# Optimization experiments

Measured on AMD Instinct MI355X. Metric: run time of the kernel, lower is better.

## Reference

```python
import jax, jax.numpy as jnp
import numpy as np

B, C, H, W = 4, 256, 128, 128
HEADS, KD, VD = 8, 64, 64
EPS = 1e-5


def setup_inputs() -> dict:
    key = jax.random.key(0)
    ks = jax.random.split(key, 5)
    s = 0.02
    return {
        "x": jax.random.normal(ks[0], (B, C, H, W), dtype=jnp.float32),
        "wq": jax.random.normal(ks[1], (HEADS * KD, C), dtype=jnp.float32) * s,
        "bq": jnp.zeros((HEADS * KD,), dtype=jnp.float32),
        "wk": jax.random.normal(ks[2], (HEADS * KD, C), dtype=jnp.float32) * s,
        "bk": jnp.zeros((HEADS * KD,), dtype=jnp.float32),
        "wv": jax.random.normal(ks[3], (HEADS * VD, C), dtype=jnp.float32) * s,
        "bv": jnp.zeros((HEADS * VD,), dtype=jnp.float32),
        "wo": jax.random.normal(ks[4], (C, HEADS * VD), dtype=jnp.float32) * s,
        "bo": jnp.zeros((C,), dtype=jnp.float32),
        "g_q": jnp.ones((KD,), dtype=jnp.float32),
        "be_q": jnp.zeros((KD,), dtype=jnp.float32),
        "g_k": jnp.ones((KD,), dtype=jnp.float32),
        "be_k": jnp.zeros((KD,), dtype=jnp.float32),
        "g_v": jnp.ones((VD,), dtype=jnp.float32),
        "be_v": jnp.zeros((VD,), dtype=jnp.float32),
    }


def _conv1x1(t, w, b):
    # t: [B,C,H,W], w: [O,C] -> [B,O,H,W]
    return jnp.einsum("bchw,oc->bohw", t, w) + b[None, :, None, None]


def _ln_dim(t, g, be):
    # LayerNorm over the per-head feature axis (axis=2) of [B,heads,dim,N]
    mu = jnp.mean(t, axis=2, keepdims=True)
    var = jnp.var(t, axis=2, keepdims=True)
    return (t - mu) * jax.lax.rsqrt(var + EPS) * g[None, None, :, None] + be[None, None, :, None]


def reference(x, wq, bq, wk, bk, wv, bv, wo, bo, g_q, be_q, g_k, be_k, g_v, be_v):
    b, c, h, w = x.shape
    n = h * w
    # context defaults to x
    q = _conv1x1(x, wq, bq).reshape(b, HEADS, KD, n)
    k = _conv1x1(x, wk, bk).reshape(b, HEADS, KD, n)
    v = _conv1x1(x, wv, bv).reshape(b, HEADS, VD, n)
    q = _ln_dim(q, g_q, be_q)
    k = _ln_dim(k, g_k, be_k)
    v = _ln_dim(v, g_v, be_v)
    q = jax.nn.softmax(q * (KD ** -0.25), axis=2)  # softmax over key_dim
    k = jax.nn.softmax(k, axis=3)                  # softmax over N
    ctx = jnp.einsum("bhkn,bhvn->bhkv", k, v)      # [B,heads,KD,VD]
    out = jnp.einsum("bhkn,bhkv->bhvn", q, ctx)    # [B,heads,VD,N]
    out = out.reshape(b, HEADS * VD, h, w)
    return _conv1x1(out, wo, bo)
```

## Files before the change

### kernel.cpp

```cpp
#include <hip/hip_runtime.h>
#include <hip/hip_bf16.h>
#include <stdint.h>

typedef unsigned short u16;
typedef __attribute__((__vector_size__(16))) short s16x8;
typedef __attribute__((__vector_size__(16))) float f32x4;

#define N_ 16384
#define C_ 256

__device__ __forceinline__ float bf2f(u16 u) {
    union { uint32_t i; float f; } v; v.i = ((uint32_t)u) << 16; return v.f;
}
__device__ __forceinline__ u16 f2bf(float f) {
    union { uint32_t i; float f; } v; v.f = f;
    uint32_t u = v.i;
    return (u16)((u + 0x7FFFu + ((u >> 16) & 1u)) >> 16);
}

__device__ __forceinline__ void gl_lds16(const u16* g, u16* l) {
    __builtin_amdgcn_global_load_lds((__attribute__((address_space(1))) void*)g,
                                     (__attribute__((address_space(3))) void*)l,
                                     16, 0, 0);
}

__global__ __launch_bounds__(256) void transpose_kernel(const float* __restrict__ x,
                                                        u16* __restrict__ xT) {
    __shared__ float T[64][65];
    int tid = threadIdx.x;
    int n0 = blockIdx.x * 64, c0 = blockIdx.y * 64, b = blockIdx.z;
    const float* xp = x + (size_t)b * C_ * N_;
    for (int it = 0; it < 16; it++) {
        int idx = it * 256 + tid;
        int c = idx >> 6, n = idx & 63;
        T[c][n] = xp[(size_t)(c0 + c) * N_ + n0 + n];
    }
    __syncthreads();
    u16* op = xT + (size_t)b * N_ * C_;
    for (int it = 0; it < 8; it++) {
        int idx = it * 256 + tid;
        int n = idx >> 5, c2 = (idx & 31) * 2;
        uint32_t lo = f2bf(T[c2][n]);
        uint32_t hi = f2bf(T[c2 + 1][n]);
        *(uint32_t*)&op[(size_t)(n0 + n) * C_ + c0 + c2] = lo | (hi << 16);
    }
}

__global__ __launch_bounds__(256) void cvtw_kernel(const float* __restrict__ wq,
                                                   const float* __restrict__ wk,
                                                   const float* __restrict__ wv,
                                                   u16* __restrict__ wb,
                                                   float* __restrict__ rs) {
    int m = blockIdx.y;
    if (m == 0 && blockIdx.x < 8) rs[blockIdx.x * 256 + threadIdx.x] = 0.f;
    const float* s = m == 0 ? wq : (m == 1 ? wk : wv);
    int i = blockIdx.x * 256 + threadIdx.x;
    wb[(size_t)m * 131072 + i] = f2bf(s[i]);
}


__global__ __launch_bounds__(256) void kvctx_kernel(
    const u16* __restrict__ xT, const u16* __restrict__ wb,
    const float* __restrict__ bk, const float* __restrict__ bv,
    const float* __restrict__ gk, const float* __restrict__ bek,
    const float* __restrict__ gv, const float* __restrict__ bev,
    float* __restrict__ ctxp, float* __restrict__ rs)
{
    __shared__ u16 SH[4][8704];
    int tid = threadIdx.x;
    int lane = tid & 63, wid = tid >> 6;
    int quad = lane >> 4, l15 = lane & 15;
    int wm = wid >> 1, wn = wid & 1;
    int ns = blockIdx.x, h = blockIdx.y, b = blockIdx.z;

    const u16* wsrcw = wb + (size_t)(1 + (wid >> 1)) * 131072
                          + ((size_t)h * 64 + (size_t)(wid & 1) * 32) * 256;

    int srow = lane >> 3;
    int sc8  = ((lane & 7) ^ srow) * 8;

#define STAGEF(XP, KC, CUR) {                                                      \
    int koff_ = (KC) * 64 + sc8;                                                   \
    _Pragma("unroll")                                                              \
    for (int i_ = 0; i_ < 4; i_++) {                                               \
        int ri_ = i_ * 8 + srow;                                                   \
        gl_lds16(&wsrcw[(size_t)ri_ * 256 + koff_], &SH[CUR][(wid * 4 + i_) * 512]); \
        gl_lds16(&(XP)[(size_t)(wid * 32 + ri_) * 256 + koff_], &SH[2 + (CUR)][(wid * 4 + i_) * 512]); \
    } }

    const float* bptr  = wm ? bv  : bk;
    const float* gptr  = wm ? gv  : gk;
    const float* beptr = wm ? bev : bek;
    float bB_[4], gB[4], eB[4];
#pragma unroll
    for (int nf = 0; nf < 4; nf++) {
        int rl = nf * 16 + l15;
        bB_[nf] = bptr[h * 64 + rl];
        gB[nf]  = gptr[rl];
        eB[nf]  = beptr[rl];
    }

    f32x4 cacc[4][4];
#pragma unroll
    for (int i = 0; i < 4; i++)
#pragma unroll
        for (int j = 0; j < 4; j++) cacc[i][j] = (f32x4){0.f, 0.f, 0.f, 0.f};
    float rs_acc[4] = {0.f, 0.f, 0.f, 0.f};

    {
        const u16* x0 = xT + ((size_t)b * N_ + (size_t)(ns * 8) * 128) * 256;
        STAGEF(x0, 0, 0);
    }
    __syncthreads();

    for (int t = 0; t < 8; t++) {
        const u16* xcur = xT + ((size_t)b * N_ + (size_t)(ns * 8 + t) * 128) * 256;

        f32x4 acc[4][4];
#pragma unroll
        for (int i = 0; i < 4; i++)
#pragma unroll
            for (int j = 0; j < 4; j++) acc[i][j] = (f32x4){0.f, 0.f, 0.f, 0.f};

        for (int kc = 0; kc < 4; kc++) {
            int cur = (kc + t) & 1;
            if (kc < 3) STAGEF(xcur, kc + 1, cur ^ 1);
            const u16* Wb = &SH[cur][0];
            const u16* Xb = &SH[2 + cur][0];
#pragma unroll
            for (int ks = 0; ks < 2; ks++) {
                int cc = ks * 4 + quad;
                s16x8 af[4], bf[4];
#pragma unroll
                for (int f = 0; f < 4; f++) {
                    int ar = wn * 64 + f * 16 + l15;
                    int br = wm * 64 + f * 16 + l15;
                    af[f] = *(const s16x8*)&Xb[ar * 64 + ((cc ^ (ar & 7)) * 8)];
                    bf[f] = *(const s16x8*)&Wb[br * 64 + ((cc ^ (br & 7)) * 8)];
                }
#pragma unroll
                for (int i = 0; i < 4; i++)
#pragma unroll
                    for (int j = 0; j < 4; j++)
                        acc[i][j] = __builtin_amdgcn_mfma_f32_16x16x32_bf16(af[i], bf[j], acc[i][j], 0, 0, 0);
            }
            if (kc < 3) __syncthreads();
        }

#pragma unroll
        for (int mf = 0; mf < 4; mf++)
#pragma unroll
            for (int nf = 0; nf < 4; nf++)
#pragma unroll
                for (int r = 0; r < 4; r++) acc[mf][nf][r] += bB_[nf];
        float sa[4][4], sb[4][4];
#pragma unroll
        for (int mf = 0; mf < 4; mf++)
#pragma unroll
            for (int r = 0; r < 4; r++) {
                float s = 0.f, s2 = 0.f;
#pragma unroll
                for (int nf = 0; nf < 4; nf++) { float v = acc[mf][nf][r]; s += v; s2 += v * v; }
                sa[mf][r] = s; sb[mf][r] = s2;
            }
#pragma unroll
        for (int msk = 1; msk <= 8; msk <<= 1)
#pragma unroll
            for (int mf = 0; mf < 4; mf++)
#pragma unroll
                for (int r = 0; r < 4; r++) {
                    sa[mf][r] += __shfl_xor(sa[mf][r], msk);
                    sb[mf][r] += __shfl_xor(sb[mf][r], msk);
                }
#pragma unroll
        for (int mf = 0; mf < 4; mf++)
#pragma unroll
            for (int r = 0; r < 4; r++) {
                float mu = sa[mf][r] * (1.f / 64.f);
                float rstd = rsqrtf(sb[mf][r] * (1.f / 64.f) - mu * mu + 1e-5f);
#pragma unroll
                for (int nf = 0; nf < 4; nf++)
                    acc[mf][nf][r] = (acc[mf][nf][r] - mu) * rstd * gB[nf] + eB[nf];
            }
        if (wm == 0) {
#pragma unroll
            for (int mf = 0; mf < 4; mf++)
#pragma unroll
                for (int nf = 0; nf < 4; nf++)
#pragma unroll
                    for (int r = 0; r < 4; r++) acc[mf][nf][r] = __expf(acc[mf][nf][r]);
#pragma unroll
            for (int nf = 0; nf < 4; nf++) {
                float s = 0.f;
#pragma unroll
                for (int mf = 0; mf < 4; mf++)
#pragma unroll
                    for (int r = 0; r < 4; r++) s += acc[mf][nf][r];
                s += __shfl_xor(s, 16); s += __shfl_xor(s, 32);
                rs_acc[nf] += s;
            }
        }

        int esb = t & 1;
        u16* ES = &SH[esb][0];
        u16* VS = &SH[2 + esb][0];
        {
            u16* st = wm ? VS : ES;
#pragma unroll
            for (int mf = 0; mf < 4; mf++)
#pragma unroll
                for (int nf = 0; nf < 4; nf++) {
                    int rh = nf * 16 + l15;
                    int ln = wn * 64 + mf * 16 + quad * 4;
                    int c  = ln >> 3;
                    int off = rh * 128 + ((c ^ (rh & 15)) * 8) + (ln & 7);
                    uint64_t w0 = (uint64_t)f2bf(acc[mf][nf][0]) | ((uint64_t)f2bf(acc[mf][nf][1]) << 16) |
                                  ((uint64_t)f2bf(acc[mf][nf][2]) << 32) | ((uint64_t)f2bf(acc[mf][nf][3]) << 48);
                    *(uint64_t*)&st[off] = w0;
                }
        }
        __syncthreads();

        if (t < 7) {
            const u16* xnext = xT + ((size_t)b * N_ + (size_t)(ns * 8 + t + 1) * 128) * 256;
            STAGEF(xnext, 0, (t + 1) & 1);
        }
        {
            int cc = wid * 4 + quad;
            s16x8 caf[4], cbf[4];
#pragma unroll
            for (int f = 0; f < 4; f++) {
                int off = (f * 16 + l15) * 128 + ((cc ^ l15) * 8);
                caf[f] = *(const s16x8*)&ES[off];
                cbf[f] = *(const s16x8*)&VS[off];
            }
#pragma unroll
            for (int i = 0; i < 4; i++)
#pragma unroll
                for (int j = 0; j < 4; j++)
                    cacc[i][j] = __builtin_amdgcn_mfma_f32_16x16x32_bf16(caf[i], cbf[j], cacc[i][j], 0, 0, 0);
        }
        __syncthreads();
    }

    if (wm == 0 && quad == 0) {
#pragma unroll
        for (int nf = 0; nf < 4; nf++)
            atomicAdd(&rs[(size_t)b * 512 + h * 64 + nf * 16 + l15], rs_acc[nf]);
    }
    {
        float* CTXW = (float*)((char*)SH + (size_t)wid * 17408);
#pragma unroll
        for (int mf = 0; mf < 4; mf++)
#pragma unroll
            for (int nf = 0; nf < 4; nf++) {
                int kd = mf * 16 + quad * 4, vd = nf * 16 + l15;
                *(f32x4*)&CTXW[vd * 68 + kd] = cacc[mf][nf];
            }
    }
    __syncthreads();
    {
        int vd = tid >> 2, kd0 = (tid & 3) * 16;
        const float* C0 = (const float*)((char*)SH);
        const float* C1 = (const float*)((char*)SH + 17408);
        const float* C2 = (const float*)((char*)SH + 34816);
        const float* C3 = (const float*)((char*)SH + 52224);
        float* gp = ctxp + (((size_t)(b * 8 + h) * 16 + ns) * 4096) + vd * 64 + kd0;
#pragma unroll
        for (int j4 = 0; j4 < 4; j4++) {
            int o = vd * 68 + kd0 + j4 * 4;
            f32x4 s = *(const f32x4*)&C0[o];
            s += *(const f32x4*)&C1[o];
            s += *(const f32x4*)&C2[o];
            s += *(const f32x4*)&C3[o];
            *(f32x4*)&gp[j4 * 4] = s;
        }
    }
#undef STAGEF
}

__global__ __launch_bounds__(256) void weff_kernel(
    const float* __restrict__ ctxp, const float* __restrict__ rs,
    const float* __restrict__ wo, u16* __restrict__ Weffb)
{
    __shared__ float CT[16][65];
    int tid = threadIdx.x;
    int h = blockIdx.x, b = blockIdx.y, kc = blockIdx.z;
    for (int i = tid; i < 1024; i += 256) {
        int kdl = i >> 6, vd = i & 63;
        int kd = kc * 16 + kdl;
        float s = 0.f;
#pragma unroll
        for (int sl = 0; sl < 16; sl++)
            s += ctxp[(((size_t)(b * 8 + h) * 16 + sl) * 4096) + vd * 64 + kd];
        CT[kdl][vd] = s / rs[(size_t)b * 512 + h * 64 + kd];
    }
    __syncthreads();
    int c = tid;
    float wrow[64];
    const float4* wp = (const float4*)(wo + (size_t)c * 512 + h * 64);
#pragma unroll
    for (int i = 0; i < 16; i++) { float4 t = wp[i]; wrow[i*4] = t.x; wrow[i*4+1] = t.y; wrow[i*4+2] = t.z; wrow[i*4+3] = t.w; }
    for (int kdl = 0; kdl < 16; kdl++) {
        float s = 0.f;
#pragma unroll
        for (int vd = 0; vd < 64; vd++) s += wrow[vd] * CT[kdl][vd];
        Weffb[((size_t)b * 256 + c) * 512 + h * 64 + kc * 16 + kdl] = f2bf(s);
    }
}

__global__ __launch_bounds__(256) void qout_kernel(
    const u16* __restrict__ xT, const u16* __restrict__ wb,
    const float* __restrict__ bq, const float* __restrict__ gq, const float* __restrict__ beq,
    const u16* __restrict__ Weffb, const float* __restrict__ bo, float* __restrict__ out)
{
    __shared__ u16 WS[2][8192];
    __shared__ u16 QB[2][8192];
    int tid = threadIdx.x;
    int lane = tid & 63, wid = tid >> 6;
    int quad = lane >> 4, l15 = lane & 15;
    int wm = wid >> 1, wn = wid & 1;
    int nt = blockIdx.x, b = blockIdx.y;
    int n0 = nt * 128;

    const u16* xsrc = xT + ((size_t)b * N_ + n0) * 256;
    int srow = lane >> 3;
    int sc8  = ((lane & 7) ^ srow) * 8;

    f32x4 oacc[8][4];
#pragma unroll
    for (int i = 0; i < 8; i++)
#pragma unroll
        for (int j = 0; j < 4; j++) oacc[i][j] = (f32x4){0.f, 0.f, 0.f, 0.f};

#define QSTAGE(WSRC, KC, CUR) {                                                    \
    int koff_ = (KC) * 64 + sc8;                                                   \
    _Pragma("unroll")                                                              \
    for (int i_ = 0; i_ < 4; i_++) {                                               \
        int row_ = (wid * 4 + i_) * 8 + srow;                                      \
        gl_lds16(&(WSRC)[(size_t)row_ * 256 + koff_], &WS[CUR][(wid * 4 + i_) * 512]);  \
        gl_lds16(&xsrc[(size_t)row_ * 256 + koff_], &QB[CUR][(wid * 4 + i_) * 512]);    \
    } }

    for (int p = 0; p < 4; p++) {
        const u16* wsrc = wb + (size_t)(p * 128) * 256;
        f32x4 qacc[4][4];
#pragma unroll
        for (int i = 0; i < 4; i++)
#pragma unroll
            for (int j = 0; j < 4; j++) qacc[i][j] = (f32x4){0.f, 0.f, 0.f, 0.f};

        QSTAGE(wsrc, 0, 0);
        __syncthreads();
        for (int kc = 0; kc < 4; kc++) {
            int cur = kc & 1;
            if (kc < 3) QSTAGE(wsrc, kc + 1, cur ^ 1);
            const u16* Wb = &WS[cur][0];
            const u16* Xb = &QB[cur][0];
#pragma unroll
            for (int ks = 0; ks < 2; ks++) {
                int cc = ks * 4 + quad;
                s16x8 af[4], bf[4];
#pragma unroll
                for (int f = 0; f < 4; f++) {
                    int ar = wm * 64 + f * 16 + l15;
                    int br = wn * 64 + f * 16 + l15;
                    af[f] = *(const s16x8*)&Wb[ar * 64 + ((cc ^ (ar & 7)) * 8)];
                    bf[f] = *(const s16x8*)&Xb[br * 64 + ((cc ^ (br & 7)) * 8)];
                }
#pragma unroll
                for (int i = 0; i < 4; i++)
#pragma unroll
                    for (int j = 0; j < 4; j++)
                        qacc[i][j] = __builtin_amdgcn_mfma_f32_16x16x32_bf16(af[i], bf[j], qacc[i][j], 0, 0, 0);
            }
            if (kc < 3) __syncthreads();
        }

        int r0 = p * 128;
        float bA[4][4], gA[4][4], eA[4][4];
#pragma unroll
        for (int mf = 0; mf < 4; mf++)
#pragma unroll
            for (int r = 0; r < 4; r++) {
                int rl = mf * 16 + quad * 4 + r;
                bA[mf][r] = bq[r0 + wm * 64 + rl];
                gA[mf][r] = gq[rl];
                eA[mf][r] = beq[rl];
            }
#pragma unroll
        for (int mf = 0; mf < 4; mf++)
#pragma unroll
            for (int nf = 0; nf < 4; nf++)
#pragma unroll
                for (int r = 0; r < 4; r++) qacc[mf][nf][r] += bA[mf][r];
#pragma unroll
        for (int nf = 0; nf < 4; nf++) {
            float s = 0.f, s2 = 0.f;
#pragma unroll
            for (int mf = 0; mf < 4; mf++)
#pragma unroll
                for (int r = 0; r < 4; r++) { float v = qacc[mf][nf][r]; s += v; s2 += v * v; }
            s  += __shfl_xor(s, 16);  s  += __shfl_xor(s, 32);
            s2 += __shfl_xor(s2, 16); s2 += __shfl_xor(s2, 32);
            float mu = s * (1.f / 64.f);
            float rstd = rsqrtf(s2 * (1.f / 64.f) - mu * mu + 1e-5f);
#pragma unroll
            for (int mf = 0; mf < 4; mf++)
#pragma unroll
                for (int r = 0; r < 4; r++)
                    qacc[mf][nf][r] = (qacc[mf][nf][r] - mu) * rstd * gA[mf][r] + eA[mf][r];
        }
        const float s_q = 0.35355339059327373f;
#pragma unroll
        for (int nf = 0; nf < 4; nf++) {
            float m = -1e30f;
#pragma unroll
            for (int mf = 0; mf < 4; mf++)
#pragma unroll
                for (int r = 0; r < 4; r++) { qacc[mf][nf][r] *= s_q; m = fmaxf(m, qacc[mf][nf][r]); }
            m = fmaxf(m, __shfl_xor(m, 16)); m = fmaxf(m, __shfl_xor(m, 32));
            float d = 0.f;
#pragma unroll
            for (int mf = 0; mf < 4; mf++)
#pragma unroll
                for (int r = 0; r < 4; r++) { float e = __expf(qacc[mf][nf][r] - m); qacc[mf][nf][r] = e; d += e; }
            d += __shfl_xor(d, 16); d += __shfl_xor(d, 32);
            float inv = 1.f / d;
#pragma unroll
            for (int mf = 0; mf < 4; mf++)
#pragma unroll
                for (int r = 0; r < 4; r++) qacc[mf][nf][r] *= inv;
        }
        __syncthreads();
        {
            u16* st = &QB[wn][0];
#pragma unroll
            for (int mf = 0; mf < 4; mf++)
#pragma unroll
                for (int nf = 0; nf < 4; nf++) {
                    int nl = nf * 16 + l15;
                    int gl = wm * 64 + mf * 16 + quad * 4;
                    int c  = gl >> 3;
                    int off = nl * 128 + ((c ^ (nl & 15)) * 8) + (gl & 7);
                    uint64_t w0 = (uint64_t)f2bf(qacc[mf][nf][0]) | ((uint64_t)f2bf(qacc[mf][nf][1]) << 16) |
                                  ((uint64_t)f2bf(qacc[mf][nf][2]) << 32) | ((uint64_t)f2bf(qacc[mf][nf][3]) << 48);
                    *(uint64_t*)&st[off] = w0;
                }
        }
        __syncthreads();

#pragma unroll
        for (int sub = 0; sub < 2; sub++) {
#pragma unroll
            for (int i_ = 0; i_ < 8; i_++) {
                int row = wid * 64 + i_ * 8 + srow;
                gl_lds16(&Weffb[((size_t)b * 256 + row) * 512 + p * 128 + sub * 64 + sc8],
                         &WS[wid >> 1][((wid & 1) * 64 + i_ * 8) * 64]);
            }
            __syncthreads();
#pragma unroll
            for (int ks = 0; ks < 2; ks++) {
                int cca = ks * 4 + quad;
                int ccb = sub * 8 + ks * 4 + quad;
                s16x8 af[8], bf[4];
#pragma unroll
                for (int f = 0; f < 8; f++) {
                    int ar = f * 16 + l15;
                    af[f] = *(const s16x8*)&WS[wm][ar * 64 + ((cca ^ (ar & 7)) * 8)];
                }
#pragma unroll
                for (int f = 0; f < 4; f++) {
                    int br = f * 16 + l15;
                    bf[f] = *(const s16x8*)&QB[wn][br * 128 + ((ccb ^ (br & 15)) * 8)];
                }
#pragma unroll
                for (int i = 0; i < 8; i++)
#pragma unroll
                    for (int j = 0; j < 4; j++)
                        oacc[i][j] = __builtin_amdgcn_mfma_f32_16x16x32_bf16(af[i], bf[j], oacc[i][j], 0, 0, 0);
            }
            __syncthreads();
        }
    }
#undef QSTAGE

#pragma unroll
    for (int mf = 0; mf < 8; mf++)
#pragma unroll
        for (int r = 0; r < 4; r++) {
            int c = wm * 128 + mf * 16 + quad * 4 + r;
            float bov = bo[c];
#pragma unroll
            for (int nf = 0; nf < 4; nf++)
                out[((size_t)b * 256 + c) * N_ + n0 + wn * 64 + nf * 16 + l15] = oacc[mf][nf][r] + bov;
        }
}

extern "C" void kernel_launch(void* const* d_in, const int* in_sizes, int n_in,
                              void* d_out, int out_size, void* d_ws, size_t ws_size,
                              hipStream_t stream) {
    const float* x   = (const float*)d_in[0];
    const float* wq  = (const float*)d_in[1];
    const float* bq  = (const float*)d_in[2];
    const float* wk  = (const float*)d_in[3];
    const float* bk  = (const float*)d_in[4];
    const float* wv  = (const float*)d_in[5];
    const float* bv  = (const float*)d_in[6];
    const float* wo  = (const float*)d_in[7];
    const float* bo  = (const float*)d_in[8];
    const float* gq  = (const float*)d_in[9];
    const float* beq = (const float*)d_in[10];
    const float* gk  = (const float*)d_in[11];
    const float* bek = (const float*)d_in[12];
    const float* gv  = (const float*)d_in[13];
    const float* bev = (const float*)d_in[14];
    float* out = (float*)d_out;

    char* ws = (char*)d_ws;
    u16* xT      = (u16*)(ws);
    u16* wb      = (u16*)(ws + 33554432ULL);
    float* ctxp  = (float*)(ws + 101449728ULL);
    float* rs    = (float*)(ws + 169082880ULL);
    u16* Weffb   = (u16*)(ws + 169091072ULL);

    cvtw_kernel<<<dim3(512, 3), 256, 0, stream>>>(wq, wk, wv, wb, rs);
    transpose_kernel<<<dim3(256, 4, 4), 256, 0, stream>>>(x, xT);

    kvctx_kernel<<<dim3(16, 8, 4), 256, 0, stream>>>(
        xT, wb, bk, bv, gk, bek, gv, bev, ctxp, rs);

    weff_kernel<<<dim3(8, 4, 4), 256, 0, stream>>>(ctxp, rs, wo, Weffb);

    qout_kernel<<<dim3(128, 4), 256, 0, stream>>>(xT, wb, bq, gq, beq, Weffb, bo, out);
}
```

Baseline: 346.4 us.

## Shrink kvctx LDS, read K/V weights from global, split context across waves

```diff
diff --git a/kernel.cpp b/kernel.cpp
--- a/kernel.cpp
+++ b/kernel.cpp
@@ -66,26 +66,24 @@
     const float* __restrict__ gv, const float* __restrict__ bev,
     float* __restrict__ ctxp, float* __restrict__ rs)
 {
-    __shared__ u16 SH[4][8704];
+    __shared__ u16 XS[2][8192];
     int tid = threadIdx.x;
     int lane = tid & 63, wid = tid >> 6;
     int quad = lane >> 4, l15 = lane & 15;
     int wm = wid >> 1, wn = wid & 1;
     int ns = blockIdx.x, h = blockIdx.y, b = blockIdx.z;
 
-    const u16* wsrcw = wb + (size_t)(1 + (wid >> 1)) * 131072
-                          + ((size_t)h * 64 + (size_t)(wid & 1) * 32) * 256;
+    const u16* wkb = wb + (size_t)(1 + wm) * 131072 + (size_t)h * 64 * 256;
 
     int srow = lane >> 3;
     int sc8  = ((lane & 7) ^ srow) * 8;
 
-#define STAGEF(XP, KC, CUR) {                                                      \
+#define XSTAGE(XP, KC, SLAB) {                                                     \
     int koff_ = (KC) * 64 + sc8;                                                   \
     _Pragma("unroll")                                                              \
     for (int i_ = 0; i_ < 4; i_++) {                                               \
         int ri_ = i_ * 8 + srow;                                                   \
-        gl_lds16(&wsrcw[(size_t)ri_ * 256 + koff_], &SH[CUR][(wid * 4 + i_) * 512]); \
-        gl_lds16(&(XP)[(size_t)(wid * 32 + ri_) * 256 + koff_], &SH[2 + (CUR)][(wid * 4 + i_) * 512]); \
+        gl_lds16(&(XP)[(size_t)(wid * 32 + ri_) * 256 + koff_], &XS[SLAB][(wid * 4 + i_) * 512]); \
     } }
 
     const float* bptr  = wm ? bv  : bk;
@@ -100,21 +98,21 @@
         eB[nf]  = beptr[rl];
     }
 
-    f32x4 cacc[4][4];
-#pragma unroll
-    for (int i = 0; i < 4; i++)
-#pragma unroll
-        for (int j = 0; j < 4; j++) cacc[i][j] = (f32x4){0.f, 0.f, 0.f, 0.f};
+    f32x4 cacc[2][2];
+#pragma unroll
+    for (int i = 0; i < 2; i++)
+#pragma unroll
+        for (int j = 0; j < 2; j++) cacc[i][j] = (f32x4){0.f, 0.f, 0.f, 0.f};
     float rs_acc[4] = {0.f, 0.f, 0.f, 0.f};
 
     {
-        const u16* x0 = xT + ((size_t)b * N_ + (size_t)(ns * 8) * 128) * 256;
-        STAGEF(x0, 0, 0);
+        const u16* x0 = xT + ((size_t)b * N_ + (size_t)(ns * 4) * 128) * 256;
+        XSTAGE(x0, 0, 0);
     }
     __syncthreads();
 
-    for (int t = 0; t < 8; t++) {
-        const u16* xcur = xT + ((size_t)b * N_ + (size_t)(ns * 8 + t) * 128) * 256;
+    for (int t = 0; t < 4; t++) {
+        const u16* xcur = xT + ((size_t)b * N_ + (size_t)(ns * 4 + t) * 128) * 256;
 
         f32x4 acc[4][4];
 #pragma unroll
@@ -123,10 +121,8 @@
             for (int j = 0; j < 4; j++) acc[i][j] = (f32x4){0.f, 0.f, 0.f, 0.f};
 
         for (int kc = 0; kc < 4; kc++) {
-            int cur = (kc + t) & 1;
-            if (kc < 3) STAGEF(xcur, kc + 1, cur ^ 1);
-            const u16* Wb = &SH[cur][0];
-            const u16* Xb = &SH[2 + cur][0];
+            if (kc < 3) XSTAGE(xcur, kc + 1, (kc + 1) & 1);
+            const u16* Xb = &XS[kc & 1][0];
 #pragma unroll
             for (int ks = 0; ks < 2; ks++) {
                 int cc = ks * 4 + quad;
@@ -134,9 +130,11 @@
 #pragma unroll
                 for (int f = 0; f < 4; f++) {
                     int ar = wn * 64 + f * 16 + l15;
-                    int br = wm * 64 + f * 16 + l15;
                     af[f] = *(const s16x8*)&Xb[ar * 64 + ((cc ^ (ar & 7)) * 8)];
-                    bf[f] = *(const s16x8*)&Wb[br * 64 + ((cc ^ (br & 7)) * 8)];
+                }
+#pragma unroll
+                for (int f = 0; f < 4; f++) {
+                    bf[f] = *(const s16x8*)&wkb[(size_t)(f * 16 + l15) * 256 + kc * 64 + cc * 8];
                 }
 #pragma unroll
                 for (int i = 0; i < 4; i++)
@@ -201,11 +199,10 @@
             }
         }
 
-        int esb = t & 1;
-        u16* ES = &SH[esb][0];
-        u16* VS = &SH[2 + esb][0];
+        __syncthreads();
+
         {
-            u16* st = wm ? VS : ES;
+            u16* st = wm ? &XS[1][0] : &XS[0][0];
 #pragma unroll
             for (int mf = 0; mf < 4; mf++)
 #pragma unroll
@@ -221,24 +218,34 @@
         }
         __syncthreads();
 
-        if (t < 7) {
-            const u16* xnext = xT + ((size_t)b * N_ + (size_t)(ns * 8 + t + 1) * 128) * 256;
-            STAGEF(xnext, 0, (t + 1) & 1);
-        }
         {
-            int cc = wid * 4 + quad;
-            s16x8 caf[4], cbf[4];
-#pragma unroll
-            for (int f = 0; f < 4; f++) {
-                int off = (f * 16 + l15) * 128 + ((cc ^ l15) * 8);
-                caf[f] = *(const s16x8*)&ES[off];
-                cbf[f] = *(const s16x8*)&VS[off];
-            }
-#pragma unroll
-            for (int i = 0; i < 4; i++)
-#pragma unroll
-                for (int j = 0; j < 4; j++)
-                    cacc[i][j] = __builtin_amdgcn_mfma_f32_16x16x32_bf16(caf[i], cbf[j], cacc[i][j], 0, 0, 0);
+            const u16* ES = &XS[0][0];
+            const u16* VS = &XS[1][0];
+#pragma unroll
+            for (int cc = 0; cc < 4; cc++) {
+                s16x8 caf[2], cbf[2];
+#pragma unroll
+                for (int f = 0; f < 2; f++) {
+                    int rh = wm * 32 + f * 16 + l15;
+                    caf[f] = *(const s16x8*)&ES[rh * 128 + (((cc * 4 + quad) ^ (rh & 15)) * 8)];
+                }
+#pragma unroll
+                for (int f = 0; f < 2; f++) {
+                    int rh = wn * 32 + f * 16 + l15;
+                    cbf[f] = *(const s16x8*)&VS[rh * 128 + (((cc * 4 + quad) ^ (rh & 15)) * 8)];
+                }
+#pragma unroll
+                for (int i = 0; i < 2; i++)
+#pragma unroll
+                    for (int j = 0; j < 2; j++)
+                        cacc[i][j] = __builtin_amdgcn_mfma_f32_16x16x32_bf16(caf[i], cbf[j], cacc[i][j], 0, 0, 0);
+            }
+        }
+        __syncthreads();
+
+        if (t < 3) {
+            const u16* xnext = xT + ((size_t)b * N_ + (size_t)(ns * 4 + t + 1) * 128) * 256;
+            XSTAGE(xnext, 0, 0);
         }
         __syncthreads();
     }
@@ -249,34 +256,17 @@
             atomicAdd(&rs[(size_t)b * 512 + h * 64 + nf * 16 + l15], rs_acc[nf]);
     }
     {
-        float* CTXW = (float*)((char*)SH + (size_t)wid * 17408);
-#pragma unroll
-        for (int mf = 0; mf < 4; mf++)
-#pragma unroll
-            for (int nf = 0; nf < 4; nf++) {
-                int kd = mf * 16 + quad * 4, vd = nf * 16 + l15;
-                *(f32x4*)&CTXW[vd * 68 + kd] = cacc[mf][nf];
-            }
-    }
-    __syncthreads();
-    {
-        int vd = tid >> 2, kd0 = (tid & 3) * 16;
-        const float* C0 = (const float*)((char*)SH);
-        const float* C1 = (const float*)((char*)SH + 17408);
-        const float* C2 = (const float*)((char*)SH + 34816);
-        const float* C3 = (const float*)((char*)SH + 52224);
-        float* gp = ctxp + (((size_t)(b * 8 + h) * 16 + ns) * 4096) + vd * 64 + kd0;
-#pragma unroll
-        for (int j4 = 0; j4 < 4; j4++) {
-            int o = vd * 68 + kd0 + j4 * 4;
-            f32x4 s = *(const f32x4*)&C0[o];
-            s += *(const f32x4*)&C1[o];
-            s += *(const f32x4*)&C2[o];
-            s += *(const f32x4*)&C3[o];
-            *(f32x4*)&gp[j4 * 4] = s;
-        }
-    }
-#undef STAGEF
+        float* gp = ctxp + (((size_t)(b * 8 + h) * 32 + ns) * 4096);
+#pragma unroll
+        for (int mf = 0; mf < 2; mf++)
+#pragma unroll
+            for (int nf = 0; nf < 2; nf++) {
+                int kd = wm * 32 + mf * 16 + quad * 4;
+                int vd = wn * 32 + nf * 16 + l15;
+                *(f32x4*)&gp[vd * 64 + kd] = cacc[mf][nf];
+            }
+    }
+#undef XSTAGE
 }
 
 __global__ __launch_bounds__(256) void weff_kernel(
@@ -291,8 +281,8 @@
         int kd = kc * 16 + kdl;
         float s = 0.f;
 #pragma unroll
-        for (int sl = 0; sl < 16; sl++)
-            s += ctxp[(((size_t)(b * 8 + h) * 16 + sl) * 4096) + vd * 64 + kd];
+        for (int sl = 0; sl < 32; sl++)
+            s += ctxp[(((size_t)(b * 8 + h) * 32 + sl) * 4096) + vd * 64 + kd];
         CT[kdl][vd] = s / rs[(size_t)b * 512 + h * 64 + kd];
     }
     __syncthreads();
@@ -527,7 +517,7 @@
     cvtw_kernel<<<dim3(512, 3), 256, 0, stream>>>(wq, wk, wv, wb, rs);
     transpose_kernel<<<dim3(256, 4, 4), 256, 0, stream>>>(x, xT);
 
-    kvctx_kernel<<<dim3(16, 8, 4), 256, 0, stream>>>(
+    kvctx_kernel<<<dim3(32, 8, 4), 256, 0, stream>>>(
         xT, wb, bk, bv, gk, bek, gv, bev, ctxp, rs);
 
     weff_kernel<<<dim3(8, 4, 4), 256, 0, stream>>>(ctxp, rs, wo, Weffb);
```

Measured after the change: 370.0 us. 1.07x slower.
